# Kernel optimization log

Hardware: AMD Instinct MI355X
Metric: run time of the kernel (lower is better)

## Reference

```python
import jax, jax.numpy as jnp
import numpy as np

NUM_NODES = 500000
EMB = 200        # embedding_size
U = 10           # embedding_u_size
T = 4            # edge_type_count
DIM_A = 20
N_SRC = 65536
N_DST = 8192
E = 262144       # edges per edge type


def setup_inputs() -> dict:
    key = jax.random.key(0)
    ks = jax.random.split(key, 9)
    std = 1.0 / np.sqrt(EMB)
    return {
        "input_nodes": jax.random.randint(ks[0], (N_SRC,), 0, NUM_NODES),
        "output_nodes": jax.random.randint(ks[1], (N_DST,), 0, NUM_NODES),
        "edge_src": jax.random.randint(ks[2], (T, E), 0, N_SRC),
        "edge_dst": jax.random.randint(ks[3], (T, E), 0, N_DST),
        "node_embeddings": jax.random.uniform(ks[4], (NUM_NODES, EMB), jnp.float32, -1.0, 1.0),
        "node_type_embeddings": jax.random.uniform(ks[5], (NUM_NODES, T, U), jnp.float32, -1.0, 1.0),
        "trans_weights": std * jax.random.normal(ks[6], (T, U, EMB), jnp.float32),
        "trans_weights_s1": std * jax.random.normal(ks[7], (T, U, DIM_A), jnp.float32),
        "trans_weights_s2": std * jax.random.normal(ks[8], (T, DIM_A, 1), jnp.float32),
    }


def reference(input_nodes, output_nodes, edge_src, edge_dst,
              node_embeddings, node_type_embeddings,
              trans_weights, trans_weights_s1, trans_weights_s2):
    n_dst = output_nodes.shape[0]
    # gather per-type embeddings of source nodes: [N_src, T, U] -> [T, N_src, U]
    src_feat = jnp.moveaxis(node_type_embeddings[input_nodes], 1, 0)
    # per-edge-type copy_u + sum (scatter-add over dst nodes): [T, N_dst, U]
    agg = jax.vmap(lambda es, ed, f: jax.ops.segment_sum(f[es], ed, num_segments=n_dst))(
        edge_src, edge_dst, src_feat)
    nte = jnp.moveaxis(agg, 0, 1)  # [B, T, U]
    # attention scores: tanh(nte @ s1_t) @ s2_t per (node, type)
    h = jnp.tanh(jnp.einsum('btu,tua->bta', nte, trans_weights_s1))      # [B, T, A]
    scores = jnp.einsum('bta,ta->bt', h, trans_weights_s2[..., 0])        # [B, T]
    att = jax.nn.softmax(scores, axis=1)                                  # [B, T]
    # attention-weighted combine (repeat in torch makes all T rows identical)
    combined = jnp.einsum('bt,btu->bu', att, nte)                         # [B, U]
    # final per-type projection + base embedding
    out = node_embeddings[output_nodes][:, None, :] + \
        jnp.einsum('bu,tue->bte', combined, trans_weights)                # [B, T, EMB]
    # F.normalize(dim=2), eps=1e-12
    norm = jnp.linalg.norm(out, axis=2, keepdims=True)
    return out / jnp.maximum(norm, 1e-12)
```

## Files before the change

kernel.cpp:

```cpp
#include <hip/hip_runtime.h>
#include <math.h>

#define T_CNT 4
#define U_DIM 10
#define A_DIM 20
#define EMB_D 200
#define N_SRC 65536
#define N_DST 8192
#define E_PER_T 262144

#define NCHUNK 32
#define DCHUNK (N_DST / NCHUNK)
#define MAX_SEG 8

__global__ __launch_bounds__(256)
void scan_kernel(const int* __restrict__ edge_src,
                 const int* __restrict__ edge_dst,
                 const int* __restrict__ input_nodes,
                 const float* __restrict__ nte,
                 float* __restrict__ part,
                 int eseg) {
    __shared__ float acc[DCHUNK * U_DIM];

    const int b = blockIdx.x;
    const int c = b & (NCHUNK - 1);
    const int t = (b >> 5) & (T_CNT - 1);
    const int s = b >> 7;
    const int base = c * DCHUNK;

    for (int i = threadIdx.x; i < DCHUNK * U_DIM; i += 256) acc[i] = 0.f;
    __syncthreads();

    const int* ed = edge_dst + (size_t)t * E_PER_T + (size_t)s * eseg;
    const int* es = edge_src + (size_t)t * E_PER_T + (size_t)s * eseg;

    for (int k = threadIdx.x * 4; k < eseg; k += 1024) {
        int4 d4 = *reinterpret_cast<const int4*>(ed + k);
        unsigned r0 = (unsigned)(d4.x - base);
        unsigned r1 = (unsigned)(d4.y - base);
        unsigned r2 = (unsigned)(d4.z - base);
        unsigned r3 = (unsigned)(d4.w - base);
        bool p0 = r0 < DCHUNK, p1 = r1 < DCHUNK, p2 = r2 < DCHUNK, p3 = r3 < DCHUNK;
        if (p0 | p1 | p2 | p3) {
            int4 s4 = *reinterpret_cast<const int4*>(es + k);
            int srcs[4] = {s4.x, s4.y, s4.z, s4.w};
            unsigned rs[4] = {r0, r1, r2, r3};
            bool ps[4] = {p0, p1, p2, p3};
#pragma unroll
            for (int j = 0; j < 4; ++j) {
                if (ps[j]) {
                    int node = input_nodes[srcs[j]];
                    const float2* f2 = reinterpret_cast<const float2*>(
                        nte + (size_t)node * (T_CNT * U_DIM) + t * U_DIM);
                    int off = (int)rs[j] * U_DIM;
#pragma unroll
                    for (int q = 0; q < 5; ++q) {
                        float2 v = f2[q];
                        atomicAdd(&acc[off + 2 * q], v.x);
                        atomicAdd(&acc[off + 2 * q + 1], v.y);
                    }
                }
            }
        }
    }
    __syncthreads();

    float* outp = part + (((size_t)(s * T_CNT + t)) * N_DST + base) * U_DIM;
    for (int i = threadIdx.x; i < DCHUNK * U_DIM; i += 256) outp[i] = acc[i];
}

__global__ __launch_bounds__(256)
void finalize_kernel(const float* __restrict__ part,
                     const int* __restrict__ output_nodes,
                     const float* __restrict__ node_emb,
                     const float* __restrict__ W,
                     const float* __restrict__ S1,
                     const float* __restrict__ S2,
                     float* __restrict__ out,
                     int nseg) {
    const int b = blockIdx.x;
    const int tid = threadIdx.x;

    __shared__ float sNte[T_CNT * U_DIM];
    __shared__ float sH[T_CNT * A_DIM];
    __shared__ float sScore[T_CNT];
    __shared__ float sAtt[T_CNT];
    __shared__ float sComb[U_DIM];
    __shared__ float sBase[EMB_D];

    if (tid < T_CNT * U_DIM) {
        int t = tid / U_DIM, u = tid - t * U_DIM;
        float v = 0.f;
        for (int s = 0; s < nseg; ++s)
            v += part[(((size_t)(s * T_CNT + t)) * N_DST + b) * U_DIM + u];
        sNte[tid] = v;
    }
    const int on = output_nodes[b];
    if (tid < EMB_D) sBase[tid] = node_emb[(size_t)on * EMB_D + tid];
    __syncthreads();

    if (tid < T_CNT * A_DIM) {
        int t = tid / A_DIM, a = tid - t * A_DIM;
        float s = 0.f;
#pragma unroll
        for (int u = 0; u < U_DIM; ++u)
            s += sNte[t * U_DIM + u] * S1[t * (U_DIM * A_DIM) + u * A_DIM + a];
        sH[tid] = tanhf(s);
    }
    __syncthreads();

    if (tid < T_CNT) {
        float s = 0.f;
#pragma unroll
        for (int a = 0; a < A_DIM; ++a)
            s += sH[tid * A_DIM + a] * S2[tid * A_DIM + a];
        sScore[tid] = s;
    }
    __syncthreads();

    if (tid == 0) {
        float m = sScore[0];
#pragma unroll
        for (int t = 1; t < T_CNT; ++t) m = fmaxf(m, sScore[t]);
        float sum = 0.f;
#pragma unroll
        for (int t = 0; t < T_CNT; ++t) {
            float e = __expf(sScore[t] - m);
            sAtt[t] = e;
            sum += e;
        }
        float inv = 1.f / sum;
#pragma unroll
        for (int t = 0; t < T_CNT; ++t) sAtt[t] *= inv;
    }
    __syncthreads();

    if (tid < U_DIM) {
        float s = 0.f;
#pragma unroll
        for (int t = 0; t < T_CNT; ++t) s += sAtt[t] * sNte[t * U_DIM + tid];
        sComb[tid] = s;
    }
    __syncthreads();

    const int t = tid >> 6;
    const int lane = tid & 63;
    float c[U_DIM];
#pragma unroll
    for (int u = 0; u < U_DIM; ++u) c[u] = sComb[u];

    float v[4];
    float sq = 0.f;
#pragma unroll
    for (int j = 0; j < 4; ++j) {
        int e = lane + j * 64;
        if (e < EMB_D) {
            float s = sBase[e];
            const float* w = W + t * (U_DIM * EMB_D) + e;
#pragma unroll
            for (int u = 0; u < U_DIM; ++u) s += c[u] * w[u * EMB_D];
            v[j] = s;
            sq += s * s;
        }
    }
#pragma unroll
    for (int off = 32; off > 0; off >>= 1) sq += __shfl_xor(sq, off);

    float n = sqrtf(sq);
    float inv = 1.f / fmaxf(n, 1e-12f);

    float* o = out + (size_t)b * (T_CNT * EMB_D) + t * EMB_D;
#pragma unroll
    for (int j = 0; j < 4; ++j) {
        int e = lane + j * 64;
        if (e < EMB_D) o[e] = v[j] * inv;
    }
}

extern "C" void kernel_launch(void* const* d_in, const int* in_sizes, int n_in,
                              void* d_out, int out_size, void* d_ws, size_t ws_size,
                              hipStream_t stream) {
    const int*   input_nodes   = (const int*)d_in[0];
    const int*   output_nodes  = (const int*)d_in[1];
    const int*   edge_src      = (const int*)d_in[2];
    const int*   edge_dst      = (const int*)d_in[3];
    const float* node_emb      = (const float*)d_in[4];
    const float* node_type_emb = (const float*)d_in[5];
    const float* W             = (const float*)d_in[6];
    const float* S1            = (const float*)d_in[7];
    const float* S2             = (const float*)d_in[8];
    float*       out           = (float*)d_out;

    const size_t segBytes = (size_t)T_CNT * N_DST * U_DIM * sizeof(float);
    int nseg = (int)(ws_size / segBytes);
    if (nseg > MAX_SEG) nseg = MAX_SEG;
    if (nseg < 1) nseg = 1;
    while (nseg & (nseg - 1)) nseg--;
    const int eseg = E_PER_T / nseg;

    float* part = (float*)d_ws;

    scan_kernel<<<NCHUNK * T_CNT * nseg, 256, 0, stream>>>(
        edge_src, edge_dst, input_nodes, node_type_emb, part, eseg);

    finalize_kernel<<<N_DST, 256, 0, stream>>>(
        part, output_nodes, node_emb, W, S1, S2, out, nseg);
}
```

Baseline: 624.0 us.

## Pre-gather source features into compact buffer and widen dst chunks per scan block

Adds a gather kernel that copies the node_type_embeddings rows for the input nodes into a dense workspace buffer, so the scan reads features by source index instead of through a double indirection into a 500k-row table. It also cuts dst chunks from 32 to 8, so each block keeps 1024 destinations in LDS and the edge lists are re-read 4x fewer times. More edge segments (up to 32) keep the grid large. Feature loads are batched ahead of the LDS atomics to expose memory-level parallelism, at the cost of an extra kernel launch, more workspace use, and more partial sums for finalize to reduce.

```diff
diff --git a/kernel.cpp b/kernel.cpp
--- a/kernel.cpp
+++ b/kernel.cpp
@@ -9,23 +9,36 @@
 #define N_DST 8192
 #define E_PER_T 262144
 
-#define NCHUNK 32
+#define NCHUNK 8
 #define DCHUNK (N_DST / NCHUNK)
-#define MAX_SEG 8
-
+#define MAX_SEG 32
+
+__global__ __launch_bounds__(256)
+void gather_kernel(const int* __restrict__ input_nodes,
+                   const float4* __restrict__ nte4,
+                   float4* __restrict__ src_feat4) {
+    int id = blockIdx.x * 256 + threadIdx.x;
+    if (id >= N_SRC * U_DIM) return;
+    int i = id / 10;
+    int q = id - i * 10;
+    int node = input_nodes[i];
+    src_feat4[i * 10 + q] = nte4[(size_t)node * 10 + q];
+}
+
+template <bool PRE>
 __global__ __launch_bounds__(256)
 void scan_kernel(const int* __restrict__ edge_src,
                  const int* __restrict__ edge_dst,
                  const int* __restrict__ input_nodes,
-                 const float* __restrict__ nte,
+                 const float* __restrict__ feat,
                  float* __restrict__ part,
                  int eseg) {
     __shared__ float acc[DCHUNK * U_DIM];
 
     const int b = blockIdx.x;
     const int c = b & (NCHUNK - 1);
-    const int t = (b >> 5) & (T_CNT - 1);
-    const int s = b >> 7;
+    const int t = (b >> 3) & (T_CNT - 1);
+    const int s = b >> 5;
     const int base = c * DCHUNK;
 
     for (int i = threadIdx.x; i < DCHUNK * U_DIM; i += 256) acc[i] = 0.f;
@@ -36,29 +49,35 @@
 
     for (int k = threadIdx.x * 4; k < eseg; k += 1024) {
         int4 d4 = *reinterpret_cast<const int4*>(ed + k);
-        unsigned r0 = (unsigned)(d4.x - base);
-        unsigned r1 = (unsigned)(d4.y - base);
-        unsigned r2 = (unsigned)(d4.z - base);
-        unsigned r3 = (unsigned)(d4.w - base);
-        bool p0 = r0 < DCHUNK, p1 = r1 < DCHUNK, p2 = r2 < DCHUNK, p3 = r3 < DCHUNK;
-        if (p0 | p1 | p2 | p3) {
-            int4 s4 = *reinterpret_cast<const int4*>(es + k);
-            int srcs[4] = {s4.x, s4.y, s4.z, s4.w};
-            unsigned rs[4] = {r0, r1, r2, r3};
-            bool ps[4] = {p0, p1, p2, p3};
-#pragma unroll
-            for (int j = 0; j < 4; ++j) {
-                if (ps[j]) {
-                    int node = input_nodes[srcs[j]];
-                    const float2* f2 = reinterpret_cast<const float2*>(
-                        nte + (size_t)node * (T_CNT * U_DIM) + t * U_DIM);
-                    int off = (int)rs[j] * U_DIM;
-#pragma unroll
-                    for (int q = 0; q < 5; ++q) {
-                        float2 v = f2[q];
-                        atomicAdd(&acc[off + 2 * q], v.x);
-                        atomicAdd(&acc[off + 2 * q + 1], v.y);
-                    }
+        int4 s4 = *reinterpret_cast<const int4*>(es + k);
+        int dsts[4] = {d4.x, d4.y, d4.z, d4.w};
+        int srcs[4] = {s4.x, s4.y, s4.z, s4.w};
+        unsigned r[4];
+        bool p[4];
+#pragma unroll
+        for (int j = 0; j < 4; ++j) {
+            r[j] = (unsigned)(dsts[j] - base);
+            p[j] = r[j] < DCHUNK;
+        }
+        float2 vals[4][5];
+#pragma unroll
+        for (int j = 0; j < 4; ++j) {
+            if (p[j]) {
+                int row = PRE ? srcs[j] : input_nodes[srcs[j]];
+                const float2* f2 = reinterpret_cast<const float2*>(
+                    feat + (size_t)row * (T_CNT * U_DIM) + t * U_DIM);
+#pragma unroll
+                for (int q = 0; q < 5; ++q) vals[j][q] = f2[q];
+            }
+        }
+#pragma unroll
+        for (int j = 0; j < 4; ++j) {
+            if (p[j]) {
+                int off = (int)r[j] * U_DIM;
+#pragma unroll
+                for (int q = 0; q < 5; ++q) {
+                    atomicAdd(&acc[off + 2 * q],     vals[j][q].x);
+                    atomicAdd(&acc[off + 2 * q + 1], vals[j][q].y);
                 }
             }
         }
@@ -188,20 +207,35 @@
     const float* node_type_emb = (const float*)d_in[5];
     const float* W             = (const float*)d_in[6];
     const float* S1            = (const float*)d_in[7];
-    const float* S2             = (const float*)d_in[8];
+    const float* S2            = (const float*)d_in[8];
     float*       out           = (float*)d_out;
 
+    const size_t gatherBytes = (size_t)N_SRC * T_CNT * U_DIM * sizeof(float);
     const size_t segBytes = (size_t)T_CNT * N_DST * U_DIM * sizeof(float);
-    int nseg = (int)(ws_size / segBytes);
+
+    bool pre = ws_size >= gatherBytes + segBytes;
+    size_t avail = pre ? (ws_size - gatherBytes) : ws_size;
+    int nseg = (int)(avail / segBytes);
     if (nseg > MAX_SEG) nseg = MAX_SEG;
     if (nseg < 1) nseg = 1;
     while (nseg & (nseg - 1)) nseg--;
     const int eseg = E_PER_T / nseg;
 
-    float* part = (float*)d_ws;
-
-    scan_kernel<<<NCHUNK * T_CNT * nseg, 256, 0, stream>>>(
-        edge_src, edge_dst, input_nodes, node_type_emb, part, eseg);
+    float* src_feat = (float*)d_ws;
+    float* part = pre ? (float*)((char*)d_ws + gatherBytes) : (float*)d_ws;
+
+    const int grid = NCHUNK * T_CNT * nseg;
+
+    if (pre) {
+        const int n = N_SRC * U_DIM;
+        gather_kernel<<<(n + 255) / 256, 256, 0, stream>>>(
+            input_nodes, (const float4*)node_type_emb, (float4*)src_feat);
+        scan_kernel<true><<<grid, 256, 0, stream>>>(
+            edge_src, edge_dst, input_nodes, src_feat, part, eseg);
+    } else {
+        scan_kernel<false><<<grid, 256, 0, stream>>>(
+            edge_src, edge_dst, input_nodes, node_type_emb, part, eseg);
+    }
 
     finalize_kernel<<<N_DST, 256, 0, stream>>>(
         part, output_nodes, node_emb, W, S1, S2, out, nseg);
```

Measured after the change: 606.8 us. 2.8% less time.
